# Performance work log

Hardware: AMD Instinct MI355X
Metric: run time of the kernel (lower is better)

The kernel has to match this reference:

```python
import jax, jax.numpy as jnp
import numpy as np

WIN_LEN = 400
WIN_INC = 100
FFT_LEN = 512
EPSILON = float(np.finfo(np.float32).eps)


def _make_kernel():
    # periodic (fftbins=True) hamming window, matching scipy.signal.get_window
    n = np.arange(WIN_LEN)
    window = 0.54 - 0.46 * np.cos(2.0 * np.pi * n / WIN_LEN)
    # direct-DFT basis: rfft of identity, truncated to win_len taps
    fourier_basis = np.fft.rfft(np.eye(FFT_LEN))[:WIN_LEN]          # [win_len, fft_len//2+1]
    kernel = np.concatenate([fourier_basis.real, fourier_basis.imag], axis=1).T  # [2*(fft//2+1), win_len]
    kernel = kernel * window                                        # window applied per tap
    return kernel[:, None, :].astype(np.float32)                    # [514, 1, 400] (OIH)


def setup_inputs() -> dict:
    key = jax.random.key(0)
    inputs = jax.random.normal(key, (16, 160000), dtype=jnp.float32)  # [B, L] waveform
    weight = jnp.asarray(_make_kernel())                              # fixed DFT buffer
    return {"inputs": inputs, "weight": weight}


def reference(inputs, weight):
    pad = WIN_LEN - WIN_INC  # 300
    x = inputs[:, None, :]                                   # [B, 1, L]
    x = jnp.pad(x, ((0, 0), (0, 0), (pad, pad)))             # symmetric pad, as in F.pad
    out = jax.lax.conv_general_dilated(
        x, weight,
        window_strides=(WIN_INC,),
        padding='VALID',
        dimension_numbers=('NCH', 'OIH', 'NCH'),
    )                                                        # [B, 514, T]
    r, i = jnp.split(out, 2, axis=1)                         # real / imag halves [B, 257, T]
    mags = jnp.sqrt(jnp.clip(r * r + i * i, EPSILON))
    phase = jnp.arctan2(i + EPSILON, r + EPSILON)
    return mags, phase
```

## Files before the change

### kernel.cpp

```cpp
#include <hip/hip_runtime.h>
#include <math.h>


#define BATCH 16
#define NSAMP 160000
#define NF 257
#define NT 1603
#define KLEN 400
#define INC 100
#define PADL 300
#define EPSF 1.1920928955078125e-7f
#define TAU 1e-2f

#define FPB 16
#define ZSTR 258
#define XSPAN ((FPB - 1) * INC + KLEN)
#define NTB ((NT + FPB - 1) / FPB)
#define SLOT(j, k) (16 * (j) + (((k) + (j)) & 15))

__device__ __forceinline__ float2 cmul(float2 a, float2 b) {
  return make_float2(a.x * b.x - a.y * b.y, a.x * b.y + a.y * b.x);
}

__device__ __forceinline__ void fft16_dif(float2* a) {
  const float C1 = 0.92387953251128674f;
  const float S1 = 0.38268343236508978f;
  const float R2 = 0.70710678118654752f;
  {
    const float2 W[8] = {{1.f, 0.f},  {C1, -S1},  {R2, -R2},  {S1, -C1},
                         {0.f, -1.f}, {-S1, -C1}, {-R2, -R2}, {-C1, -S1}};
    #pragma unroll
    for (int j = 0; j < 8; ++j) {
      float2 u = a[j], v = a[j + 8];
      a[j] = make_float2(u.x + v.x, u.y + v.y);
      float2 d = make_float2(u.x - v.x, u.y - v.y);
      a[j + 8] = cmul(d, W[j]);
    }
  }
  {
    const float2 W[4] = {{1.f, 0.f}, {R2, -R2}, {0.f, -1.f}, {-R2, -R2}};
    #pragma unroll
    for (int h = 0; h < 16; h += 8)
      #pragma unroll
      for (int j = 0; j < 4; ++j) {
        float2 u = a[h + j], v = a[h + j + 4];
        a[h + j] = make_float2(u.x + v.x, u.y + v.y);
        float2 d = make_float2(u.x - v.x, u.y - v.y);
        a[h + j + 4] = cmul(d, W[j]);
      }
  }
  #pragma unroll
  for (int q = 0; q < 16; q += 4) {
    float2 u0 = a[q], v0 = a[q + 2];
    a[q] = make_float2(u0.x + v0.x, u0.y + v0.y);
    a[q + 2] = make_float2(u0.x - v0.x, u0.y - v0.y);
    float2 u1 = a[q + 1], v1 = a[q + 3];
    a[q + 1] = make_float2(u1.x + v1.x, u1.y + v1.y);
    float2 d = make_float2(u1.x - v1.x, u1.y - v1.y);
    a[q + 3] = make_float2(d.y, -d.x);
  }
  #pragma unroll
  for (int q = 0; q < 16; q += 2) {
    float2 u = a[q], v = a[q + 1];
    a[q] = make_float2(u.x + v.x, u.y + v.y);
    a[q + 1] = make_float2(u.x - v.x, u.y - v.y);
  }
}

__device__ __forceinline__ float fast_atan2(float y, float x) {
  float ax = fabsf(x), ay = fabsf(y);
  float mx = fmaxf(ax, ay), mn = fminf(ax, ay);
  float t = mn * __builtin_amdgcn_rcpf(fmaxf(mx, 1e-37f));
  float s = t * t;
  float p = fmaf(s, -0.01172120f, 0.05265332f);
  p = fmaf(s, p, -0.11643287f);
  p = fmaf(s, p, 0.19354346f);
  p = fmaf(s, p, -0.33262347f);
  p = fmaf(s, p, 0.99997726f);
  float r = t * p;
  if (ay > ax) r = 1.57079632679489662f - r;
  if (x < 0.f) r = 3.14159265358979324f - r;
  return (y < 0.f) ? -r : r;
}

__device__ __forceinline__ void emit_fp(float rr, float ii, int ff,
                                        const float* __restrict__ w,
                                        const float* xf,
                                        float* __restrict__ out,
                                        long o, long plane) {
  float ie = ii + EPSF, re = rr + EPSF;
  if (fabsf(ie) < TAU && re < TAU) {
    const float* wr = w + (long)ff * KLEN;
    const float* wi = w + (long)(257 + ff) * KLEN;
    float r2 = 0.f, i2 = 0.f;
    for (int k = 0; k < KLEN; ++k) {
      float xv = xf[k];
      r2 = fmaf(wr[k], xv, r2);
      i2 = fmaf(wi[k], xv, i2);
    }
    rr = r2; ii = i2;
  }
  out[o] = sqrtf(fmaxf(rr * rr + ii * ii, EPSF));
  out[o + plane] = fast_atan2(ii + EPSF, rr + EPSF);
}

__global__ __launch_bounds__(256, 4)
void stft_fft10(const float* __restrict__ x, const float* __restrict__ w,
                float* __restrict__ out) {
  __shared__ float2 Z[FPB * ZSTR];
  __shared__ __align__(16) float xs[XSPAN];

  const int tid = threadIdx.x;
  const int b = blockIdx.y;
  const int tl = tid & 15;
  const int th = tid >> 4;

  const int u = blockIdx.x;
  const int xcd = u & 7;
  const int tb = ((xcd < 5) ? xcd * 13 : 65 + (xcd - 5) * 12) + (u >> 3);
  const int t0 = tb * FPB;

  const long xb = (long)b * NSAMP;
  const int base = t0 * INC - PADL;
  for (int r = 0; r < 2; ++r) {
    int i4 = r * 256 + tid;
    if (4 * i4 < XSPAN) {
      int g = base + 4 * i4;
      float4 v;
      if (g >= 0 && g + 3 < NSAMP) {
        v = *(const float4*)(x + xb + g);
      } else {
        v.x = (g + 0 >= 0 && g + 0 < NSAMP) ? x[xb + g + 0] : 0.f;
        v.y = (g + 1 >= 0 && g + 1 < NSAMP) ? x[xb + g + 1] : 0.f;
        v.z = (g + 2 >= 0 && g + 2 < NSAMP) ? x[xb + g + 2] : 0.f;
        v.w = (g + 3 >= 0 && g + 3 < NSAMP) ? x[xb + g + 3] : 0.f;
      }
      *(float4*)&xs[4 * i4] = v;
    }
  }
  __syncthreads();

  float2 a[16];
  const float* xf = &xs[tl * INC];
  #pragma unroll
  for (int n1 = 0; n1 < 12; ++n1) {
    int n = 32 * n1 + 2 * th;
    float2 xv = *(const float2*)&xf[n];
    float w0 = fmaf(-0.46f, cospif((float)n * 0.005f), 0.54f);
    float w1 = fmaf(-0.46f, cospif((float)(n + 1) * 0.005f), 0.54f);
    a[n1] = make_float2(xv.x * w0, xv.y * w1);
  }
  {
    int n = 384 + 2 * th;
    if (n < KLEN) {
      float2 xv = *(const float2*)&xf[n];
      float w0 = fmaf(-0.46f, cospif((float)n * 0.005f), 0.54f);
      float w1 = fmaf(-0.46f, cospif((float)(n + 1) * 0.005f), 0.54f);
      a[12] = make_float2(xv.x * w0, xv.y * w1);
    } else {
      a[12] = make_float2(0.f, 0.f);
    }
  }
  a[13] = a[14] = a[15] = make_float2(0.f, 0.f);

  fft16_dif(a);

  static const int BR[16] = {0, 8, 4, 12, 2, 10, 6, 14,
                             1, 9, 5, 13, 3, 11, 7, 15};
  float2* Zf = Z + tl * ZSTR;
  #pragma unroll
  for (int r = 0; r < 16; ++r) {
    const int k1 = BR[r];
    float2 v;
    if (k1 == 0) {
      v = a[r];
    } else {
      float aa = (float)(th * k1) * (1.0f / 128.0f);
      float2 t256 = make_float2(cospif(aa), -sinpif(aa));
      v = cmul(a[r], t256);
    }
    Zf[SLOT(th, k1)] = v;
  }
  __syncthreads();

  {
    float2 g[16];
    #pragma unroll
    for (int n2 = 0; n2 < 16; ++n2) g[n2] = Zf[SLOT(n2, th)];
    fft16_dif(g);
    #pragma unroll
    for (int r = 0; r < 16; ++r) {
      const int k2 = BR[r];
      Zf[SLOT(k2, th)] = g[r];
    }
  }
  __syncthreads();

  const long plane = (long)BATCH * NF * NT;
  const long pb = (long)b * NF * NT;
  for (int r = 0; r < 9; ++r) {
    int tau = r * 256 + tid;
    if (tau < FPB * 129) {
      int t16 = tau & 15;
      int p = tau >> 4;
      float2* Zt = Z + t16 * ZSTR;
      int q = (256 - p) & 255;
      float2 z0 = Zt[SLOT(p >> 4, p & 15)];
      float2 z1 = Zt[SLOT(q >> 4, q & 15)];
      float2 ze = make_float2(0.5f * (z0.x + z1.x), 0.5f * (z0.y - z1.y));
      float2 zo = make_float2(0.5f * (z0.y + z1.y), 0.5f * (z1.x - z0.x));
      float ta = (float)p * (1.0f / 256.0f);
      float2 T = make_float2(cospif(ta), -sinpif(ta));
      float2 tz = cmul(zo, T);
      float2 ya = make_float2(ze.x + tz.x, ze.y + tz.y);
      float2 yb = make_float2(ze.x - tz.x, tz.y - ze.y);
      int tt = t0 + t16;
      if (tt < NT) {
        const float* xfr = &xs[t16 * INC];
        emit_fp(ya.x, ya.y, p, w, xfr, out, pb + (long)p * NT + tt, plane);
        if (p == 0) {
          emit_fp(yb.x, 0.f, 256, w, xfr, out,
                  pb + (long)256 * NT + tt, plane);
        } else {
          emit_fp(yb.x, yb.y, 256 - p, w, xfr, out,
                  pb + (long)(256 - p) * NT + tt, plane);
        }
      }
    }
  }
}

extern "C" void kernel_launch(void* const* d_in, const int* in_sizes, int n_in,
                              void* d_out, int out_size, void* d_ws, size_t ws_size,
                              hipStream_t stream) {
  const float* x = (const float*)d_in[0];
  const float* w = (const float*)d_in[1];
  float* out = (float*)d_out;

  dim3 grid(NTB, BATCH);
  stft_fft10<<<grid, dim3(256), 0, stream>>>(x, w, out);
}
```

Baseline: 156.6 us.

## Do real-FFT post-processing in registers via wave shuffles instead of shared memory

Swaps the thread-to-frame mapping so the 16 threads sharing a frame sit within one wavefront. The second FFT stage's outputs then stay in registers, and the conjugate-pair partner for the real-FFT split is fetched with __shfl rather than through a shared-memory round trip. This drops one barrier and a set of LDS reads and writes, and replaces the per-bin cospif/sinpif twiddles with a constant table times one per-thread twiddle. Each thread now emits 16 bins directly, which changes the output store pattern (bins now vary across lanes for a fixed frame) and may reduce coalescing.

```diff
diff --git a/kernel.cpp b/kernel.cpp
--- a/kernel.cpp
+++ b/kernel.cpp
@@ -105,15 +105,15 @@
 }
 
 __global__ __launch_bounds__(256, 4)
-void stft_fft10(const float* __restrict__ x, const float* __restrict__ w,
+void stft_fft11(const float* __restrict__ x, const float* __restrict__ w,
                 float* __restrict__ out) {
   __shared__ float2 Z[FPB * ZSTR];
   __shared__ __align__(16) float xs[XSPAN];
 
   const int tid = threadIdx.x;
   const int b = blockIdx.y;
-  const int tl = tid & 15;
-  const int th = tid >> 4;
+  const int th = tid & 15;
+  const int fi = tid >> 4;
 
   const int u = blockIdx.x;
   const int xcd = u & 7;
@@ -141,7 +141,7 @@
   __syncthreads();
 
   float2 a[16];
-  const float* xf = &xs[tl * INC];
+  const float* xf = &xs[fi * INC];
   #pragma unroll
   for (int n1 = 0; n1 < 12; ++n1) {
     int n = 32 * n1 + 2 * th;
@@ -167,7 +167,7 @@
 
   static const int BR[16] = {0, 8, 4, 12, 2, 10, 6, 14,
                              1, 9, 5, 13, 3, 11, 7, 15};
-  float2* Zf = Z + tl * ZSTR;
+  float2* Zf = Z + fi * ZSTR;
   #pragma unroll
   for (int r = 0; r < 16; ++r) {
     const int k1 = BR[r];
@@ -176,55 +176,64 @@
       v = a[r];
     } else {
       float aa = (float)(th * k1) * (1.0f / 128.0f);
-      float2 t256 = make_float2(cospif(aa), -sinpif(aa));
-      v = cmul(a[r], t256);
+      v = cmul(a[r], make_float2(cospif(aa), -sinpif(aa)));
     }
     Zf[SLOT(th, k1)] = v;
   }
   __syncthreads();
 
-  {
-    float2 g[16];
-    #pragma unroll
-    for (int n2 = 0; n2 < 16; ++n2) g[n2] = Zf[SLOT(n2, th)];
-    fft16_dif(g);
-    #pragma unroll
-    for (int r = 0; r < 16; ++r) {
-      const int k2 = BR[r];
-      Zf[SLOT(k2, th)] = g[r];
-    }
-  }
-  __syncthreads();
+  float2 g[16];
+  #pragma unroll
+  for (int n2 = 0; n2 < 16; ++n2) g[n2] = Zf[SLOT(n2, th)];
+  fft16_dif(g);
+
+  static const int P0R[16] = {0, 1, 3, 2, 7, 6, 5, 4,
+                              15, 14, 13, 12, 11, 10, 9, 8};
+  static const float2 CK[16] = {
+    {1.f, 0.f},
+    {0.98078528040323044913f, -0.19509032201612826785f},
+    {0.92387953251128675613f, -0.38268343236508977173f},
+    {0.83146961230254523708f, -0.55557023301960222474f},
+    {0.70710678118654752440f, -0.70710678118654752440f},
+    {0.55557023301960222474f, -0.83146961230254523708f},
+    {0.38268343236508977173f, -0.92387953251128675613f},
+    {0.19509032201612826785f, -0.98078528040323044913f},
+    {0.f, -1.f},
+    {-0.19509032201612826785f, -0.98078528040323044913f},
+    {-0.38268343236508977173f, -0.92387953251128675613f},
+    {-0.55557023301960222474f, -0.83146961230254523708f},
+    {-0.70710678118654752440f, -0.70710678118654752440f},
+    {-0.83146961230254523708f, -0.55557023301960222474f},
+    {-0.92387953251128675613f, -0.38268343236508977173f},
+    {-0.98078528040323044913f, -0.19509032201612826785f}};
+
+  const int lane = tid & 63;
+  const int pl = ((16 - th) & 15) | (lane & 48);
+  float tha = (float)th * (1.0f / 256.0f);
+  float2 Tth = make_float2(cospif(tha), -sinpif(tha));
 
   const long plane = (long)BATCH * NF * NT;
   const long pb = (long)b * NF * NT;
-  for (int r = 0; r < 9; ++r) {
-    int tau = r * 256 + tid;
-    if (tau < FPB * 129) {
-      int t16 = tau & 15;
-      int p = tau >> 4;
-      float2* Zt = Z + t16 * ZSTR;
-      int q = (256 - p) & 255;
-      float2 z0 = Zt[SLOT(p >> 4, p & 15)];
-      float2 z1 = Zt[SLOT(q >> 4, q & 15)];
+  const int tt = t0 + fi;
+
+  #pragma unroll
+  for (int r = 0; r < 16; ++r) {
+    const int k2 = BR[r];
+    float2 z0 = g[r];
+    float2 zsh = make_float2(__shfl(g[15 - r].x, pl),
+                             __shfl(g[15 - r].y, pl));
+    float2 z1 = (th == 0) ? g[P0R[r]] : zsh;
+    if (tt < NT) {
+      const int p = 16 * k2 + th;
+      float2 T = cmul(Tth, CK[k2]);
       float2 ze = make_float2(0.5f * (z0.x + z1.x), 0.5f * (z0.y - z1.y));
       float2 zo = make_float2(0.5f * (z0.y + z1.y), 0.5f * (z1.x - z0.x));
-      float ta = (float)p * (1.0f / 256.0f);
-      float2 T = make_float2(cospif(ta), -sinpif(ta));
       float2 tz = cmul(zo, T);
-      float2 ya = make_float2(ze.x + tz.x, ze.y + tz.y);
-      float2 yb = make_float2(ze.x - tz.x, tz.y - ze.y);
-      int tt = t0 + t16;
-      if (tt < NT) {
-        const float* xfr = &xs[t16 * INC];
-        emit_fp(ya.x, ya.y, p, w, xfr, out, pb + (long)p * NT + tt, plane);
-        if (p == 0) {
-          emit_fp(yb.x, 0.f, 256, w, xfr, out,
-                  pb + (long)256 * NT + tt, plane);
-        } else {
-          emit_fp(yb.x, yb.y, 256 - p, w, xfr, out,
-                  pb + (long)(256 - p) * NT + tt, plane);
-        }
+      emit_fp(ze.x + tz.x, ze.y + tz.y, p, w, xf, out,
+              pb + (long)p * NT + tt, plane);
+      if (th == 0 && r == 0) {
+        emit_fp(z0.x - z0.y, 0.f, 256, w, xf, out,
+                pb + (long)256 * NT + tt, plane);
       }
     }
   }
@@ -238,5 +247,5 @@
   float* out = (float*)d_out;
 
   dim3 grid(NTB, BATCH);
-  stft_fft10<<<grid, dim3(256), 0, stream>>>(x, w, out);
-}
+  stft_fft11<<<grid, dim3(256), 0, stream>>>(x, w, out);
+}
```

Result: slower. 186.8 us (+19.3%).
